# Kernel optimization log

Measured on AMD Instinct MI355X. Metric: run time of the kernel, lower is better.

Reference implementation:

```python
import jax, jax.numpy as jnp
import numpy as np
import math

B, S, DM, H = 2, 2048, 1024, 16
DH = DM // H  # 64


def setup_inputs() -> dict:
    key = jax.random.key(0)
    ks = jax.random.split(key, 12)
    s = 1.0 / math.sqrt(DM)
    inp = {
        "key": jax.random.normal(ks[0], (B, S, DM), jnp.float32),
        "value": jax.random.normal(ks[1], (B, S, DM), jnp.float32),
        "query": jax.random.normal(ks[2], (B, S, DM), jnp.float32),
        # causal mask: True = masked out (matches masked_fill semantics)
        "mask": jnp.broadcast_to(~jnp.tril(jnp.ones((S, S), bool)), (B, S, S)),
        "Wk": jax.random.normal(ks[3], (DM, DM), jnp.float32) * s,
        "bk": jnp.zeros((DM,), jnp.float32),
        "Wv": jax.random.normal(ks[4], (DM, DM), jnp.float32) * s,
        "bv": jnp.zeros((DM,), jnp.float32),
        "Wq": jax.random.normal(ks[5], (DM, DM), jnp.float32) * s,
        "bq": jnp.zeros((DM,), jnp.float32),
        "Wo": jax.random.normal(ks[6], (DM, DM), jnp.float32) * s,
        "bo": jnp.zeros((DM,), jnp.float32),
    }
    return inp


def _split_heads(x):
    # [B, S, H*DH] -> [B, H, S, DH]
    b, s, _ = x.shape
    return x.reshape(b, s, H, DH).transpose(0, 2, 1, 3)


def reference(key, value, query, mask, Wk, bk, Wv, bv, Wq, bq, Wo, bo):
    key_up = _split_heads(key @ Wk.T + bk)      # [B,H,S,DH]
    value_up = _split_heads(value @ Wv.T + bv)  # [B,H,S,DH]
    query_up = _split_heads(query @ Wq.T + bq) / math.sqrt(DH)
    scores = jnp.einsum("bhqd,bhkd->bhqk", query_up, key_up)  # [B,H,S,S]
    scores = jnp.where(mask[:, None, :, :], jnp.float32(-1e18), scores)
    attn = jax.nn.softmax(scores, axis=-1)
    # dropout is identity in eval mode
    context = jnp.einsum("bhqk,bhkd->bhqd", attn, value_up)
    context = context.transpose(0, 2, 1, 3).reshape(key.shape[0], -1, H * DH)
    output = context @ Wo.T + bo                # [B,S,DM]
    top_attn = attn[:, 0, :, :]                 # [B,S,S]
    return output, top_attn
```

## Files before the change

kernel.cpp:

```cpp
#include <hip/hip_runtime.h>
#include <hip/hip_bf16.h>
#include <math.h>

#define B_ 2
#define S_ 2048
#define DM_ 1024
#define H_ 16
#define DH_ 64

using short8 = __attribute__((ext_vector_type(8))) short;
using f32x4  = __attribute__((ext_vector_type(4))) float;

typedef const __attribute__((address_space(1))) void* gas_cvp;
typedef __attribute__((address_space(3))) void* las_vp;

struct CvtJobs {
    const float* in[7];
    ushort* out[7];
};

__device__ __forceinline__ ushort f2bu(float x) {
    __hip_bfloat16 h = __float2bfloat16(x);
    return *(ushort*)&h;
}

__global__ __launch_bounds__(256) void cvt_bf16(CvtJobs jobs) {
    const int bid = blockIdx.x;
    int j, blk;
    if (bid < 6144) { j = bid >> 11; blk = bid & 2047; }
    else { const int r = bid - 6144; j = 3 + (r >> 9); blk = r & 511; }
    const int idx = (blk * 256 + threadIdx.x) * 8;
    const float* in = jobs.in[j];
    float4 a = *(const float4*)&in[idx];
    float4 b = *(const float4*)&in[idx + 4];
    ushort u[8];
    u[0] = f2bu(a.x); u[1] = f2bu(a.y); u[2] = f2bu(a.z); u[3] = f2bu(a.w);
    u[4] = f2bu(b.x); u[5] = f2bu(b.y); u[6] = f2bu(b.z); u[7] = f2bu(b.w);
    *(int4*)&jobs.out[j][idx] = *(int4*)u;
}

#define GEMM_STAGE(buf, k0v)                                                   \
    {                                                                          \
        _Pragma("unroll")                                                      \
        for (int i = 0; i < 2; i++) {                                          \
            const int s   = i * 256 + tid;                                     \
            const int c   = s >> 7;                                            \
            const int row = s & 127;                                           \
            __builtin_amdgcn_global_load_lds(                                  \
                (gas_cvp)(Ag + (size_t)(i0 + row) * 1024 + (k0v) + c * 8),     \
                (las_vp)&AsB[buf][0][(i * 256 + w * 64) * 8], 16, 0, 0);       \
            __builtin_amdgcn_global_load_lds(                                  \
                (gas_cvp)(Wg + (size_t)(j0 + row) * 1024 + (k0v) + c * 8),     \
                (las_vp)&AsB[buf][1][(i * 256 + w * 64) * 8], 16, 0, 0);       \
        }                                                                      \
    }

#define GEMM_KLOOP()                                                           \
    {                                                                          \
        int bufc = 0;                                                          \
        GEMM_STAGE(0, 0);                                                      \
        GEMM_STAGE(1, 32);                                                     \
        for (int k0 = 0; k0 < 1024; k0 += 32) {                                \
            if (k0 + 32 < 1024)                                                \
                asm volatile("s_waitcnt vmcnt(4)" ::: "memory");               \
            else                                                               \
                asm volatile("s_waitcnt vmcnt(0)" ::: "memory");               \
            __builtin_amdgcn_s_barrier();                                      \
            if (k0 + 64 < 1024) {                                              \
                const int nb = (bufc + 2 >= 3) ? bufc - 1 : bufc + 2;          \
                GEMM_STAGE(nb, k0 + 64);                                       \
            }                                                                  \
            short8 af[4], bf[4];                                               \
            _Pragma("unroll")                                                  \
            for (int m = 0; m < 4; m++)                                        \
                af[m] = *(const short8*)&AsB[bufc][0][((g << 7) + wm * 64 + m * 16 + lr) * 8]; \
            _Pragma("unroll")                                                  \
            for (int n = 0; n < 4; n++)                                        \
                bf[n] = *(const short8*)&AsB[bufc][1][((g << 7) + wn * 64 + n * 16 + lr) * 8]; \
            _Pragma("unroll")                                                  \
            for (int m = 0; m < 4; m++)                                        \
                _Pragma("unroll")                                              \
                for (int n = 0; n < 4; n++)                                    \
                    acc[m][n] = __builtin_amdgcn_mfma_f32_16x16x32_bf16(       \
                        af[m], bf[n], acc[m][n], 0, 0, 0);                     \
            bufc = (bufc + 1 == 3) ? 0 : bufc + 1;                             \
        }                                                                      \
    }

struct ProjJobs {
    const ushort* A[3];
    const ushort* W[3];
    const float* bias[3];
    ushort* C[3];
    float scale[3];
};

__global__ __launch_bounds__(256) void gemm_proj3(ProjJobs jobs)
{
    __shared__ ushort AsB[3][2][4096];

    const int o   = blockIdx.x;
    const int swz = (o & 7) * 96 + (o >> 3);
    const int z   = swz >> 8;
    const int rem = swz & 255;
    const int by  = rem >> 3;
    const int bx  = rem & 7;

    const ushort* Ag = jobs.A[z];
    const ushort* Wg = jobs.W[z];
    const float* bias = jobs.bias[z];
    ushort* C = jobs.C[z];
    const float scale = jobs.scale[z];

    const int tid  = threadIdx.x;
    const int w    = tid >> 6;
    const int lane = tid & 63;
    const int g    = lane >> 4;
    const int lr   = lane & 15;
    const int wm   = w >> 1;
    const int wn   = w & 1;
    const int i0   = by * 128;
    const int j0   = bx * 128;

    f32x4 acc[4][4];
    #pragma unroll
    for (int m = 0; m < 4; m++)
        #pragma unroll
        for (int n = 0; n < 4; n++)
            #pragma unroll
            for (int jj = 0; jj < 4; jj++) acc[m][n][jj] = 0.f;

    GEMM_KLOOP();

    const int colbase = j0 + wn * 64;
    const int rowbase = i0 + wm * 64;
    #pragma unroll
    for (int n = 0; n < 4; n++) {
        const int col = colbase + n * 16 + lr;
        const float bb = bias[col];
        const int hh = col >> 6;
        const int d = col & 63;
        #pragma unroll
        for (int m = 0; m < 4; m++) {
            const int rb = rowbase + m * 16 + g * 4;
            #pragma unroll
            for (int jj = 0; jj < 4; jj++) {
                const float v = (acc[m][n][jj] + bb) * scale;
                const int i = rb + jj;
                const int b = i >> 11;
                const int srow = i & 2047;
                C[(((size_t)b * H_ + hh) * S_ + srow) * DH_ + d] = f2bu(v);
            }
        }
    }
}

__global__ __launch_bounds__(512) void flash_mfma(
    const ushort* __restrict__ Qb, const ushort* __restrict__ Kb,
    const ushort* __restrict__ Vb, __hip_bfloat16* __restrict__ ctx,
    float* __restrict__ m0, float* __restrict__ l0)
{
    const int bid = blockIdx.x;
    const int xcd = bid & 7;
    const int t   = bid >> 3;
    const int P   = (t >> 3) * 8 + xcd;
    const int p   = t & 7;
    const int h   = P & 15;
    const int b   = P >> 4;

    const size_t hoff = ((size_t)b * H_ + h) * S_ * DH_;
    const ushort* Qh = Qb + hoff;
    const ushort* Kh = Kb + hoff;
    const ushort* Vh = Vb + hoff;

    __shared__ ushort Ks[64][72];
    __shared__ ushort Vt[64][72];
    __shared__ ushort Ps[8][16][72];

    const int tid  = threadIdx.x;
    const int w    = tid >> 6;
    const int lane = tid & 63;
    const int g    = lane >> 4;
    const int lr   = lane & 15;
    const int q0A  = p * 128 + w * 16;
    const int q0B  = (15 - p) * 128 + w * 16;
    const int diagA = (q0A + 15) >> 6;
    const int diagB = (q0B + 15) >> 6;
    const int nkt   = 2 * (16 - p);

    short8 qfA0, qfA1, qfB0, qfB1;
    {
        const ushort* qa = Qh + (size_t)(q0A + lr) * DH_ + g * 8;
        qfA0 = *(const short8*)(qa);
        qfA1 = *(const short8*)(qa + 32);
        const ushort* qb = Qh + (size_t)(q0B + lr) * DH_ + g * 8;
        qfB0 = *(const short8*)(qb);
        qfB1 = *(const short8*)(qb + 32);
    }

    f32x4 oA[4], oB[4];
    #pragma unroll
    for (int nc = 0; nc < 4; nc++) {
        oA[nc][0]=0.f; oA[nc][1]=0.f; oA[nc][2]=0.f; oA[nc][3]=0.f;
        oB[nc][0]=0.f; oB[nc][1]=0.f; oB[nc][2]=0.f; oB[nc][3]=0.f;
    }
    float mA = -1e30f, lA = 0.f;
    float mB = -1e30f, lB = 0.f;

    int4 pk = *(const int4*)(Kh + (size_t)lane * DH_ + w * 8);
    int4 pv = *(const int4*)(Vh + (size_t)lane * DH_ + w * 8);

    for (int kt = 0; kt < nkt; kt++) {
        const int kvb = kt * 64;
        __syncthreads();
        {
            *(int4*)&Ks[lane][w * 8] = pk;
            ushort vv[8];
            *(int4*)vv = pv;
            #pragma unroll
            for (int j2 = 0; j2 < 8; j2++) Vt[w * 8 + j2][lane] = vv[j2];
        }
        if (kt + 1 < nkt) {
            const size_t roff = (size_t)(kvb + 64 + lane) * DH_ + w * 8;
            pk = *(const int4*)(Kh + roff);
            pv = *(const int4*)(Vh + roff);
        }
        __syncthreads();

        #pragma unroll
        for (int u = 0; u < 2; u++) {
            const int diag = (u == 0) ? diagA : diagB;
            if (kt > diag) continue;
            const int q0w   = (u == 0) ? q0A : q0B;
            const short8 qf0 = (u == 0) ? qfA0 : qfB0;
            const short8 qf1 = (u == 0) ? qfA1 : qfB1;
            float& m_r = (u == 0) ? mA : mB;
            float& l_r = (u == 0) ? lA : lB;
            f32x4* o   = (u == 0) ? oA : oB;
            const int qglob = q0w + lr;

            f32x4 st[4];
            #pragma unroll
            for (int mt = 0; mt < 4; mt++) { st[mt][0]=0.f; st[mt][1]=0.f; st[mt][2]=0.f; st[mt][3]=0.f; }
            __builtin_amdgcn_s_setprio(1);
            #pragma unroll
            for (int mt = 0; mt < 4; mt++) {
                short8 ka = *(const short8*)&Ks[16 * mt + lr][8 * g];
                short8 kb = *(const short8*)&Ks[16 * mt + lr][32 + 8 * g];
                st[mt] = __builtin_amdgcn_mfma_f32_16x16x32_bf16(ka, qf0, st[mt], 0, 0, 0);
                st[mt] = __builtin_amdgcn_mfma_f32_16x16x32_bf16(kb, qf1, st[mt], 0, 0, 0);
            }
            __builtin_amdgcn_s_setprio(0);

            if (kt == diag) {
                #pragma unroll
                for (int mt = 0; mt < 4; mt++)
                    #pragma unroll
                    for (int jj = 0; jj < 4; jj++)
                        if (kvb + 16 * mt + 4 * g + jj > qglob) st[mt][jj] = -1e30f;
            }

            float pmax = st[0][0];
            #pragma unroll
            for (int mt = 0; mt < 4; mt++)
                #pragma unroll
                for (int jj = 0; jj < 4; jj++)
                    pmax = fmaxf(pmax, st[mt][jj]);
            pmax = fmaxf(pmax, __shfl_xor(pmax, 16));
            pmax = fmaxf(pmax, __shfl_xor(pmax, 32));

            const bool defer = __all(pmax - m_r <= 8.0f);
            float mnew = m_r, scv = 1.0f;
            if (!defer) {
                mnew = fmaxf(m_r, pmax);
                scv  = __expf(m_r - mnew);
            }

            float lsum = 0.f;
            #pragma unroll
            for (int mt = 0; mt < 4; mt++)
                #pragma unroll
                for (int jj = 0; jj < 4; jj++) {
                    st[mt][jj] = __expf(st[mt][jj] - mnew);
                    lsum += st[mt][jj];
                }
            lsum += __shfl_xor(lsum, 16);
            lsum += __shfl_xor(lsum, 32);
            l_r = l_r * scv + lsum;
            m_r = mnew;

            if (!defer) {
                float sc0 = __shfl(scv, 4 * g + 0);
                float sc1 = __shfl(scv, 4 * g + 1);
                float sc2 = __shfl(scv, 4 * g + 2);
                float sc3 = __shfl(scv, 4 * g + 3);
                #pragma unroll
                for (int nc = 0; nc < 4; nc++) {
                    o[nc][0] *= sc0; o[nc][1] *= sc1;
                    o[nc][2] *= sc2; o[nc][3] *= sc3;
                }
            }

            #pragma unroll
            for (int mt = 0; mt < 4; mt++) {
                ushort u4[4];
                #pragma unroll
                for (int jj = 0; jj < 4; jj++) u4[jj] = f2bu(st[mt][jj]);
                *(uint2*)&Ps[w][lr][16 * mt + 4 * g] = *(uint2*)u4;
            }

            short8 pa0 = *(const short8*)&Ps[w][lr][8 * g];
            short8 pa1 = *(const short8*)&Ps[w][lr][32 + 8 * g];
            __builtin_amdgcn_s_setprio(1);
            #pragma unroll
            for (int nc = 0; nc < 4; nc++) {
                short8 v0 = *(const short8*)&Vt[16 * nc + lr][8 * g];
                short8 v1 = *(const short8*)&Vt[16 * nc + lr][32 + 8 * g];
                o[nc] = __builtin_amdgcn_mfma_f32_16x16x32_bf16(pa0, v0, o[nc], 0, 0, 0);
                o[nc] = __builtin_amdgcn_mfma_f32_16x16x32_bf16(pa1, v1, o[nc], 0, 0, 0);
            }
            __builtin_amdgcn_s_setprio(0);
        }
    }

    #pragma unroll
    for (int u = 0; u < 2; u++) {
        const int q0w = (u == 0) ? q0A : q0B;
        const float m_r = (u == 0) ? mA : mB;
        const float l_r = (u == 0) ? lA : lB;
        const f32x4* o  = (u == 0) ? oA : oB;
        const float linv = 1.0f / l_r;
        float li0 = __shfl(linv, 4 * g + 0);
        float li1 = __shfl(linv, 4 * g + 1);
        float li2 = __shfl(linv, 4 * g + 2);
        float li3 = __shfl(linv, 4 * g + 3);
        #pragma unroll
        for (int reg = 0; reg < 4; reg++) {
            const int qrow = q0w + 4 * g + reg;
            const float li = (reg == 0) ? li0 : (reg == 1) ? li1 : (reg == 2) ? li2 : li3;
            __hip_bfloat16* cp = ctx + ((size_t)b * S_ + qrow) * DM_ + h * DH_;
            #pragma unroll
            for (int nc = 0; nc < 4; nc++)
                cp[16 * nc + lr] = __float2bfloat16(o[nc][reg] * li);
        }
        if (h == 0 && lane < 16) {
            m0[b * S_ + q0w + lane] = m_r;
            l0[b * S_ + q0w + lane] = l_r;
        }
    }
}

__global__ __launch_bounds__(256) void tail_fused(
    const ushort* __restrict__ ctxb, const ushort* __restrict__ Wg_,
    const float* __restrict__ bo, float* __restrict__ out,
    const ushort* __restrict__ Qb, const ushort* __restrict__ Kb,
    const float* __restrict__ m0, const float* __restrict__ l0,
    float* __restrict__ attn)
{
    __shared__ ushort AsB[3][2][4096];
    const int o = blockIdx.x;
    const int tid = threadIdx.x;
    const int w    = tid >> 6;
    const int lane = tid & 63;
    const int g    = lane >> 4;
    const int lr   = lane & 15;

    if (o < 256) {
        const int swz = (o & 7) * 32 + (o >> 3);
        const int by  = swz >> 3;
        const int bx  = swz & 7;
        const int wm  = w >> 1;
        const int wn  = w & 1;
        const int i0  = by * 128;
        const int j0  = bx * 128;
        const ushort* Ag = ctxb;
        const ushort* Wg = Wg_;

        f32x4 acc[4][4];
        #pragma unroll
        for (int m = 0; m < 4; m++)
            #pragma unroll
            for (int n = 0; n < 4; n++)
                #pragma unroll
                for (int jj = 0; jj < 4; jj++) acc[m][n][jj] = 0.f;

        GEMM_KLOOP();

        const int colbase = j0 + wn * 64;
        const int rowbase = i0 + wm * 64;
        #pragma unroll
        for (int n = 0; n < 4; n++) {
            const int col = colbase + n * 16 + lr;
            const float bb = bo[col];
            #pragma unroll
            for (int m = 0; m < 4; m++) {
                const int rb = rowbase + m * 16 + g * 4;
                #pragma unroll
                for (int jj = 0; jj < 4; jj++)
                    out[(size_t)(rb + jj) * DM_ + col] = acc[m][n][jj] + bb;
            }
        }
        return;
    }

    const int t   = o - 256;
    const int kt  = t & 31;
    const int qt2 = (t >> 5) & 31;
    const int b   = t >> 10;
    float* ap = attn + (size_t)b * S_ * S_;

    if (kt > qt2) {
        const int row = qt2 * 64 + (tid >> 2);
        const int col = kt * 64 + (tid & 3) * 16;
        float4 z = {0.f, 0.f, 0.f, 0.f};
        float* rp = ap + (size_t)row * S_ + col;
        *(float4*)&rp[0]  = z;
        *(float4*)&rp[4]  = z;
        *(float4*)&rp[8]  = z;
        *(float4*)&rp[12] = z;
        return;
    }

    ushort (*Ks)[72] = (ushort(*)[72])&AsB[0][0][0];
    const int q0w = qt2 * 64 + w * 16;
    const int kvb = kt * 64;
    const size_t hoff = (size_t)b * H_ * S_ * DH_;
    const ushort* Qh = Qb + hoff;
    const ushort* Kh = Kb + hoff;

    #pragma unroll
    for (int i = 0; i < 2; i++) {
        const int c = w + 4 * i;
        int4 k4 = *(const int4*)(Kh + (size_t)(kvb + lane) * DH_ + c * 8);
        *(int4*)&Ks[lane][c * 8] = k4;
    }

    short8 qf0, qf1;
    {
        const ushort* qp = Qh + (size_t)(q0w + lr) * DH_ + g * 8;
        qf0 = *(const short8*)(qp);
        qf1 = *(const short8*)(qp + 32);
    }
    const int qglob = q0w + lr;
    const float mv   = m0[b * S_ + qglob];
    const float linv = 1.0f / l0[b * S_ + qglob];
    __syncthreads();

    f32x4 st[4];
    #pragma unroll
    for (int mt = 0; mt < 4; mt++) { st[mt][0]=0.f; st[mt][1]=0.f; st[mt][2]=0.f; st[mt][3]=0.f; }
    #pragma unroll
    for (int mt = 0; mt < 4; mt++) {
        short8 ka = *(const short8*)&Ks[16 * mt + lr][8 * g];
        short8 kb = *(const short8*)&Ks[16 * mt + lr][32 + 8 * g];
        st[mt] = __builtin_amdgcn_mfma_f32_16x16x32_bf16(ka, qf0, st[mt], 0, 0, 0);
        st[mt] = __builtin_amdgcn_mfma_f32_16x16x32_bf16(kb, qf1, st[mt], 0, 0, 0);
    }

    float* rowp = ap + (size_t)qglob * S_ + kvb;
    #pragma unroll
    for (int mt = 0; mt < 4; mt++) {
        float4 ov;
        float v[4];
        #pragma unroll
        for (int jj = 0; jj < 4; jj++) {
            const int kv = 16 * mt + 4 * g + jj;
            float pv = __expf(st[mt][jj] - mv) * linv;
            v[jj] = (kvb + kv > qglob) ? 0.f : pv;
        }
        ov.x = v[0]; ov.y = v[1]; ov.z = v[2]; ov.w = v[3];
        *(float4*)&rowp[16 * mt + 4 * g] = ov;
    }
}

extern "C" void kernel_launch(void* const* d_in, const int* in_sizes, int n_in,
                              void* d_out, int out_size, void* d_ws, size_t ws_size,
                              hipStream_t stream)
{
    const float* key   = (const float*)d_in[0];
    const float* value = (const float*)d_in[1];
    const float* query = (const float*)d_in[2];
    const float* Wk = (const float*)d_in[4];
    const float* bk = (const float*)d_in[5];
    const float* Wv = (const float*)d_in[6];
    const float* bv = (const float*)d_in[7];
    const float* Wq = (const float*)d_in[8];
    const float* bq = (const float*)d_in[9];
    const float* Wo = (const float*)d_in[10];
    const float* bo = (const float*)d_in[11];

    char* ws = (char*)d_ws;
    const size_t per = (size_t)B_ * H_ * S_ * DH_;
    const size_t wsz = (size_t)DM_ * DM_;
    __hip_bfloat16* Qp   = (__hip_bfloat16*)ws;
    __hip_bfloat16* Kp   = Qp + per;
    __hip_bfloat16* Vp   = Kp + per;
    __hip_bfloat16* ctxb = Vp + per;
    __hip_bfloat16* qc   = ctxb + per;
    __hip_bfloat16* kc   = qc + per;
    __hip_bfloat16* vc   = kc + per;
    __hip_bfloat16* wqb  = vc + per;
    __hip_bfloat16* wkb  = wqb + wsz;
    __hip_bfloat16* wvb  = wkb + wsz;
    __hip_bfloat16* wob  = wvb + wsz;
    float* m0 = (float*)(wob + wsz);
    float* l0 = m0 + B_ * S_;

    float* out   = (float*)d_out;
    float* topat = out + (size_t)B_ * S_ * DM_;

    CvtJobs jobs;
    jobs.in[0] = query; jobs.out[0] = (ushort*)qc;
    jobs.in[1] = key;   jobs.out[1] = (ushort*)kc;
    jobs.in[2] = value; jobs.out[2] = (ushort*)vc;
    jobs.in[3] = Wq;    jobs.out[3] = (ushort*)wqb;
    jobs.in[4] = Wk;    jobs.out[4] = (ushort*)wkb;
    jobs.in[5] = Wv;    jobs.out[5] = (ushort*)wvb;
    jobs.in[6] = Wo;    jobs.out[6] = (ushort*)wob;
    cvt_bf16<<<6144 + 4 * 512, 256, 0, stream>>>(jobs);

    ProjJobs pj;
    pj.A[0] = (const ushort*)qc; pj.W[0] = (const ushort*)wqb; pj.bias[0] = bq;
    pj.C[0] = (ushort*)Qp; pj.scale[0] = 0.125f;
    pj.A[1] = (const ushort*)kc; pj.W[1] = (const ushort*)wkb; pj.bias[1] = bk;
    pj.C[1] = (ushort*)Kp; pj.scale[1] = 1.0f;
    pj.A[2] = (const ushort*)vc; pj.W[2] = (const ushort*)wvb; pj.bias[2] = bv;
    pj.C[2] = (ushort*)Vp; pj.scale[2] = 1.0f;
    gemm_proj3<<<768, 256, 0, stream>>>(pj);

    flash_mfma<<<256, 512, 0, stream>>>(
        (const ushort*)Qp, (const ushort*)Kp, (const ushort*)Vp, ctxb, m0, l0);

    tail_fused<<<256 + B_ * 32 * 32, 256, 0, stream>>>(
        (const ushort*)ctxb, (const ushort*)wob, bo, out,
        (const ushort*)Qp, (const ushort*)Kp, m0, l0, topat);
}
```

Baseline: 150.1 us.

## Split GEMM k-step into two phases and XOR-swizzle flash attention LDS tiles

```diff
diff --git a/kernel.cpp b/kernel.cpp
--- a/kernel.cpp
+++ b/kernel.cpp
@@ -39,7 +39,7 @@
     *(int4*)&jobs.out[j][idx] = *(int4*)u;
 }
 
-#define GEMM_STAGE(buf, k0v)                                                   \
+#define GEMM_STAGE_A(buf, k0v)                                                 \
     {                                                                          \
         _Pragma("unroll")                                                      \
         for (int i = 0; i < 2; i++) {                                          \
@@ -49,40 +49,64 @@
             __builtin_amdgcn_global_load_lds(                                  \
                 (gas_cvp)(Ag + (size_t)(i0 + row) * 1024 + (k0v) + c * 8),     \
                 (las_vp)&AsB[buf][0][(i * 256 + w * 64) * 8], 16, 0, 0);       \
+        }                                                                      \
+    }
+
+#define GEMM_STAGE_B(buf, k0v)                                                 \
+    {                                                                          \
+        _Pragma("unroll")                                                      \
+        for (int i = 0; i < 2; i++) {                                          \
+            const int s   = i * 256 + tid;                                     \
+            const int c   = s >> 7;                                            \
+            const int row = s & 127;                                           \
             __builtin_amdgcn_global_load_lds(                                  \
                 (gas_cvp)(Wg + (size_t)(j0 + row) * 1024 + (k0v) + c * 8),     \
                 (las_vp)&AsB[buf][1][(i * 256 + w * 64) * 8], 16, 0, 0);       \
         }                                                                      \
     }
 
-#define GEMM_KLOOP()                                                           \
+#define GEMM_KLOOP_2PH()                                                       \
     {                                                                          \
         int bufc = 0;                                                          \
-        GEMM_STAGE(0, 0);                                                      \
-        GEMM_STAGE(1, 32);                                                     \
+        GEMM_STAGE_A(0, 0);  GEMM_STAGE_B(0, 0);                               \
+        GEMM_STAGE_A(1, 32); GEMM_STAGE_B(1, 32);                              \
         for (int k0 = 0; k0 < 1024; k0 += 32) {                                \
             if (k0 + 32 < 1024)                                                \
                 asm volatile("s_waitcnt vmcnt(4)" ::: "memory");               \
             else                                                               \
                 asm volatile("s_waitcnt vmcnt(0)" ::: "memory");               \
             __builtin_amdgcn_s_barrier();                                      \
-            if (k0 + 64 < 1024) {                                              \
-                const int nb = (bufc + 2 >= 3) ? bufc - 1 : bufc + 2;          \
-                GEMM_STAGE(nb, k0 + 64);                                       \
-            }                                                                  \
-            short8 af[4], bf[4];                                               \
+            const int nb = (bufc + 2 >= 3) ? bufc - 1 : bufc + 2;              \
+            short8 af[4], bf01[2];                                             \
             _Pragma("unroll")                                                  \
             for (int m = 0; m < 4; m++)                                        \
                 af[m] = *(const short8*)&AsB[bufc][0][((g << 7) + wm * 64 + m * 16 + lr) * 8]; \
             _Pragma("unroll")                                                  \
-            for (int n = 0; n < 4; n++)                                        \
-                bf[n] = *(const short8*)&AsB[bufc][1][((g << 7) + wn * 64 + n * 16 + lr) * 8]; \
+            for (int n = 0; n < 2; n++)                                        \
+                bf01[n] = *(const short8*)&AsB[bufc][1][((g << 7) + wn * 64 + n * 16 + lr) * 8]; \
+            if (k0 + 64 < 1024) GEMM_STAGE_A(nb, k0 + 64);                     \
+            __builtin_amdgcn_s_setprio(1);                                     \
             _Pragma("unroll")                                                  \
             for (int m = 0; m < 4; m++)                                        \
                 _Pragma("unroll")                                              \
-                for (int n = 0; n < 4; n++)                                    \
+                for (int n = 0; n < 2; n++)                                    \
                     acc[m][n] = __builtin_amdgcn_mfma_f32_16x16x32_bf16(       \
-                        af[m], bf[n], acc[m][n], 0, 0, 0);                     \
+                        af[m], bf01[n], acc[m][n], 0, 0, 0);                   \
+            __builtin_amdgcn_s_setprio(0);                                     \
+            __builtin_amdgcn_s_barrier();                                      \
+            short8 bf23[2];                                                    \
+            _Pragma("unroll")                                                  \
+            for (int n = 0; n < 2; n++)                                        \
+                bf23[n] = *(const short8*)&AsB[bufc][1][((g << 7) + wn * 64 + (n + 2) * 16 + lr) * 8]; \
+            if (k0 + 64 < 1024) GEMM_STAGE_B(nb, k0 + 64);                     \
+            __builtin_amdgcn_s_setprio(1);                                     \
+            _Pragma("unroll")                                                  \
+            for (int m = 0; m < 4; m++)                                        \
+                _Pragma("unroll")                                              \
+                for (int n = 0; n < 2; n++)                                    \
+                    acc[m][n + 2] = __builtin_amdgcn_mfma_f32_16x16x32_bf16(   \
+                        af[m], bf23[n], acc[m][n + 2], 0, 0, 0);               \
+            __builtin_amdgcn_s_setprio(0);                                     \
             bufc = (bufc + 1 == 3) ? 0 : bufc + 1;                             \
         }                                                                      \
     }
@@ -130,7 +154,7 @@
             #pragma unroll
             for (int jj = 0; jj < 4; jj++) acc[m][n][jj] = 0.f;
 
-    GEMM_KLOOP();
+    GEMM_KLOOP_2PH();
 
     const int colbase = j0 + wn * 64;
     const int rowbase = i0 + wm * 64;
@@ -154,6 +178,10 @@
         }
     }
 }
+
+#define KADDR(row, cb) (KsB + (((row) << 7) + (((cb) ^ (((row) & 7) << 4)))))
+#define VADDR(row, cb) (VtB + (((row) << 7) + (((cb) ^ (((row) & 7) << 4)))))
+#define PADDR(wv, row, cb) (PsB + ((wv) << 11) + (((row) << 7) + (((cb) ^ (((row) & 7) << 4)))))
 
 __global__ __launch_bounds__(512) void flash_mfma(
     const ushort* __restrict__ Qb, const ushort* __restrict__ Kb,
@@ -173,9 +201,9 @@
     const ushort* Kh = Kb + hoff;
     const ushort* Vh = Vb + hoff;
 
-    __shared__ ushort Ks[64][72];
-    __shared__ ushort Vt[64][72];
-    __shared__ ushort Ps[8][16][72];
+    __shared__ __align__(16) char KsB[8192];
+    __shared__ __align__(16) char VtB[8192];
+    __shared__ __align__(16) char PsB[16384];
 
     const int tid  = threadIdx.x;
     const int w    = tid >> 6;
@@ -214,11 +242,12 @@
         const int kvb = kt * 64;
         __syncthreads();
         {
-            *(int4*)&Ks[lane][w * 8] = pk;
+            *(int4*)KADDR(lane, w * 16) = pk;
             ushort vv[8];
             *(int4*)vv = pv;
             #pragma unroll
-            for (int j2 = 0; j2 < 8; j2++) Vt[w * 8 + j2][lane] = vv[j2];
+            for (int j2 = 0; j2 < 8; j2++)
+                *(ushort*)VADDR(w * 8 + j2, lane * 2) = vv[j2];
         }
         if (kt + 1 < nkt) {
             const size_t roff = (size_t)(kvb + 64 + lane) * DH_ + w * 8;
@@ -245,8 +274,8 @@
             __builtin_amdgcn_s_setprio(1);
             #pragma unroll
             for (int mt = 0; mt < 4; mt++) {
-                short8 ka = *(const short8*)&Ks[16 * mt + lr][8 * g];
-                short8 kb = *(const short8*)&Ks[16 * mt + lr][32 + 8 * g];
+                short8 ka = *(const short8*)KADDR(16 * mt + lr, 16 * g);
+                short8 kb = *(const short8*)KADDR(16 * mt + lr, 64 + 16 * g);
                 st[mt] = __builtin_amdgcn_mfma_f32_16x16x32_bf16(ka, qf0, st[mt], 0, 0, 0);
                 st[mt] = __builtin_amdgcn_mfma_f32_16x16x32_bf16(kb, qf1, st[mt], 0, 0, 0);
             }
@@ -306,16 +335,16 @@
                 ushort u4[4];
                 #pragma unroll
                 for (int jj = 0; jj < 4; jj++) u4[jj] = f2bu(st[mt][jj]);
-                *(uint2*)&Ps[w][lr][16 * mt + 4 * g] = *(uint2*)u4;
-            }
-
-            short8 pa0 = *(const short8*)&Ps[w][lr][8 * g];
-            short8 pa1 = *(const short8*)&Ps[w][lr][32 + 8 * g];
+                *(uint2*)PADDR(w, lr, 32 * mt + 8 * g) = *(uint2*)u4;
+            }
+
+            short8 pa0 = *(const short8*)PADDR(w, lr, 16 * g);
+            short8 pa1 = *(const short8*)PADDR(w, lr, 64 + 16 * g);
             __builtin_amdgcn_s_setprio(1);
             #pragma unroll
             for (int nc = 0; nc < 4; nc++) {
-                short8 v0 = *(const short8*)&Vt[16 * nc + lr][8 * g];
-                short8 v1 = *(const short8*)&Vt[16 * nc + lr][32 + 8 * g];
+                short8 v0 = *(const short8*)VADDR(16 * nc + lr, 16 * g);
+                short8 v1 = *(const short8*)VADDR(16 * nc + lr, 64 + 16 * g);
                 o[nc] = __builtin_amdgcn_mfma_f32_16x16x32_bf16(pa0, v0, o[nc], 0, 0, 0);
                 o[nc] = __builtin_amdgcn_mfma_f32_16x16x32_bf16(pa1, v1, o[nc], 0, 0, 0);
             }
@@ -384,7 +413,7 @@
                 #pragma unroll
                 for (int jj = 0; jj < 4; jj++) acc[m][n][jj] = 0.f;
 
-        GEMM_KLOOP();
+        GEMM_KLOOP_2PH();
 
         const int colbase = j0 + wn * 64;
         const int rowbase = i0 + wm * 64;
```

New measurement: 140.9 us. 6.1% less time.
